# Performance work log

Measured on AMD Instinct MI355X. Metric: run time of the kernel, lower is better.

Reference implementation:

```python
import jax, jax.numpy as jnp
import numpy as np

B, CIN, H, W = 2, 3, 768, 768
CB = 32          # backbone out_channels (= channels_mid for heads)
ORDER = 5
MARGIN = 3.0     # ScaledTanh margin of refinement head


def _conv(x, w, b, pad):
    # x: [N,C,H,W], w: [O,I,kh,kw]
    y = jax.lax.conv_general_dilated(x, w, (1, 1), [(pad, pad), (pad, pad)],
                                     dimension_numbers=('NCHW', 'OIHW', 'NCHW'))
    return y + b[None, :, None, None]


def _readout(x, w1, b1, s, t, w2, b2, pad):
    # conv(k) -> batchnorm(eval, folded to scale/shift) -> relu -> dropout(eval=id) -> conv1x1
    h = _conv(x, w1, b1, pad)
    h = jax.nn.relu(h * s[None, :, None, None] + t[None, :, None, None])
    return _conv(h, w2, b2, 0)


def setup_inputs() -> dict:
    key = jax.random.key(0)
    ks = iter(jax.random.split(key, 16))
    def rn(shape, scale=0.05):
        return jax.random.normal(next(ks), shape, jnp.float32) * scale
    d = {'inputs': jax.random.normal(next(ks), (B, CIN, H, W), jnp.float32)}
    d['bb_w'] = rn((CB, CIN, 3, 3)); d['bb_b'] = jnp.zeros((CB,), jnp.float32)
    def head(name, k, cout):
        d[name + '_w1'] = rn((CB, CB, k, k)); d[name + '_b1'] = jnp.zeros((CB,), jnp.float32)
        d[name + '_s'] = jnp.ones((CB,), jnp.float32); d[name + '_t'] = jnp.zeros((CB,), jnp.float32)
        d[name + '_w2'] = rn((cout, CB, 1, 1)); d[name + '_b2'] = jnp.zeros((cout,), jnp.float32)
    head('score', 3, 2)
    head('loc', 7, 2)
    head('four', 7, ORDER * 4)
    head('ref', 7, 2)
    return d


def reference(inputs, bb_w, bb_b,
              score_w1, score_b1, score_s, score_t, score_w2, score_b2,
              loc_w1, loc_b1, loc_s, loc_t, loc_w2, loc_b2,
              four_w1, four_b1, four_s, four_t, four_w2, four_b2,
              ref_w1, ref_b1, ref_s, ref_t, ref_w2, ref_b2):
    # backbone (simple conv + relu; out_channels is an int so contour == refinement features)
    feats = jax.nn.relu(_conv(inputs, bb_w, bb_b, 1))
    scores = _readout(feats, score_w1, score_b1, score_s, score_t, score_w2, score_b2, 1)
    locations = _readout(feats, loc_w1, loc_b1, loc_s, loc_t, loc_w2, loc_b2, 3)
    fourier = _readout(feats, four_w1, four_b1, four_s, four_t, four_w2, four_b2, 3)
    # ReadOut final activation ScaledTanh(3.0), then CPNCore multiplies by internal margin 1.0;
    # feature HW == input HW (stride 1), so F.interpolate is a no-op.
    refinement = jnp.tanh(_readout(feats, ref_w1, ref_b1, ref_s, ref_t, ref_w2, ref_b2, 3)) * MARGIN
    return (scores, locations, refinement, fourier)
```

## Files before the change

### kernel.cpp

```cpp
#include <hip/hip_runtime.h>
#include <hip/hip_bf16.h>
#include <cmath>

#define HH 768
#define WW 768
#define HWSZ (768*768)

typedef __attribute__((ext_vector_type(8))) short bhalf8;
typedef __attribute__((ext_vector_type(4))) float f32x4;
typedef __attribute__((ext_vector_type(16))) float f32x16;

__device__ inline ushort f2bf(float f) {
  __hip_bfloat16 h = __float2bfloat16(f);
  return *reinterpret_cast<ushort*>(&h);
}

__global__ __launch_bounds__(256) void wxform_all_kernel(
    const float* __restrict__ w1S, const float* __restrict__ b1S,
    const float* __restrict__ sS,  const float* __restrict__ tS,
    const float* __restrict__ w1L, const float* __restrict__ b1L,
    const float* __restrict__ sL,  const float* __restrict__ tL,
    const float* __restrict__ w1F, const float* __restrict__ b1F,
    const float* __restrict__ sF,  const float* __restrict__ tF,
    const float* __restrict__ w1R, const float* __restrict__ b1R,
    const float* __restrict__ sR,  const float* __restrict__ tR,
    ushort* __restrict__ wT0, float* __restrict__ bb0, size_t wt_stride_elems)
{
  int h = blockIdx.y;
  const float *w1, *b1, *s, *t;
  int npos;
  if (h == 0)      { w1 = w1S; b1 = b1S; s = sS; t = tS; npos = 9;  }
  else if (h == 1) { w1 = w1L; b1 = b1L; s = sL; t = tL; npos = 49; }
  else if (h == 2) { w1 = w1F; b1 = b1F; s = sF; t = tF; npos = 49; }
  else             { w1 = w1R; b1 = b1R; s = sR; t = tR; npos = 49; }

  ushort* wT = wT0 + (size_t)h * wt_stride_elems;
  float*  bb = bb0 + h * 32;

  int i = blockIdx.x * 256 + threadIdx.x;
  if (i < npos * 1024) {
    int pos = i >> 10, mc = i & 1023, m = mc >> 5, c = mc & 31;
    wT[i] = f2bf(w1[(m * 32 + c) * npos + pos] * s[m]);
  }
  if (blockIdx.x == 0 && i < 32) bb[i] = b1[i] * s[i] + t[i];
}

__global__ __launch_bounds__(256) void backbone_kernel(
    const float* __restrict__ x, const float* __restrict__ w,
    const float* __restrict__ bias, ushort* __restrict__ feats)
{
  int p = blockIdx.x * 256 + threadIdx.x;
  int bb  = p / HWSZ;
  int rem = p - bb * HWSZ;
  int y   = rem / WW;
  int xx  = rem - y * WW;
  const float* xb = x + (size_t)bb * 3 * HWSZ;

  float v[3][3][3];
  #pragma unroll
  for (int c = 0; c < 3; c++)
    #pragma unroll
    for (int dy = 0; dy < 3; dy++)
      #pragma unroll
      for (int dx = 0; dx < 3; dx++) {
        int yy = y + dy - 1, xq = xx + dx - 1;
        v[c][dy][dx] = (yy >= 0 && yy < HH && xq >= 0 && xq < WW)
                         ? xb[(size_t)c * HWSZ + yy * WW + xq] : 0.f;
      }

  union { ushort u[32]; uint4 q[4]; } pk;
  #pragma unroll
  for (int o = 0; o < 32; o++) {
    float acc = bias[o];
    #pragma unroll
    for (int c = 0; c < 3; c++)
      #pragma unroll
      for (int dy = 0; dy < 3; dy++)
        #pragma unroll
        for (int dx = 0; dx < 3; dx++)
          acc = fmaf(w[((o * 3 + c) * 3 + dy) * 3 + dx], v[c][dy][dx], acc);
    pk.u[o] = f2bf(fmaxf(acc, 0.f));
  }
  uint4* dst = (uint4*)(feats + ((size_t)bb * HWSZ + rem) * 32);
  #pragma unroll
  for (int i = 0; i < 4; i++) dst[i] = pk.q[i];
}

template <int COUT, bool DO_TANH>
__device__ inline void head_epilogue(
    const f32x16 acc[2], const float* __restrict__ bbh,
    const float* __restrict__ w2, const float* __restrict__ b2,
    float* __restrict__ out_base, float* mid,
    int wv, int qr, int qc, int kg, int by, int bx, int bb)
{
  #pragma unroll
  for (int n = 0; n < 2; n++) {
    int pix = (wv * 4 + 2 * n + qr) * 16 + qc;
    #pragma unroll
    for (int rg = 0; rg < 4; rg++) {
      int m0 = 8 * rg + 4 * kg;
      f32x4 v;
      #pragma unroll
      for (int j = 0; j < 4; j++)
        v[j] = fmaxf(acc[n][rg * 4 + j] + bbh[m0 + j], 0.f);
      *(f32x4*)(mid + pix * 36 + m0) = v;
    }
  }
  __syncthreads();

  int t = threadIdx.x;
  float mv[32];
  #pragma unroll
  for (int j2 = 0; j2 < 8; j2++)
    *(f32x4*)(mv + 4 * j2) = *(const f32x4*)(mid + t * 36 + 4 * j2);

  int oy = by * 16 + (t >> 4), ox = bx * 16 + (t & 15);
  size_t opix = (size_t)oy * WW + ox;
  float* ob = out_base + (size_t)bb * COUT * HWSZ;
  #pragma unroll
  for (int oc = 0; oc < COUT; oc++) {
    float a2 = b2[oc];
    #pragma unroll
    for (int m = 0; m < 32; m++) a2 = fmaf(w2[oc * 32 + m], mv[m], a2);
    if (DO_TANH) a2 = tanhf(a2) * 3.0f;
    ob[(size_t)oc * HWSZ + opix] = a2;
  }
  __syncthreads();
}

__global__ __launch_bounds__(256, 2) void heads3_kernel(
    const ushort* __restrict__ feats,
    const ushort* __restrict__ wtL, const ushort* __restrict__ wtF,
    const ushort* __restrict__ wtR,
    const float* __restrict__ bbL, const float* __restrict__ bbF,
    const float* __restrict__ bbR,
    const float* __restrict__ w2L, const float* __restrict__ b2L,
    const float* __restrict__ w2F, const float* __restrict__ b2F,
    const float* __restrict__ w2R, const float* __restrict__ b2R,
    float* __restrict__ outL, float* __restrict__ outF, float* __restrict__ outR)
{
  __shared__ __align__(16) char smem[30976 + 28672];
  ushort* tile = (ushort*)smem;
  ushort* wrow = (ushort*)(smem + 30976);

  int bx = blockIdx.x % 48;
  int by = (blockIdx.x / 48) % 48;
  int bb = blockIdx.x / 2304;
  int x0 = bx * 16 - 3, y0 = by * 16 - 3;
  const ushort* fB = feats + (size_t)bb * HWSZ * 32;

  for (int p = threadIdx.x; p < 22 * 22; p += 256) {
    int r = p / 22, cl = p - r * 22;
    int yy = y0 + r, xx = x0 + cl;
    uint4 q0 = {0,0,0,0}, q1 = {0,0,0,0}, q2 = {0,0,0,0}, q3 = {0,0,0,0};
    if (yy >= 0 && yy < HH && xx >= 0 && xx < WW) {
      const uint4* src = (const uint4*)(fB + ((size_t)yy * WW + xx) * 32);
      q0 = src[0]; q1 = src[1]; q2 = src[2]; q3 = src[3];
    }
    ushort* dst = tile + r * 704 + cl * 8;
    *(uint4*)(dst +   0) = q0;
    *(uint4*)(dst + 176) = q1;
    *(uint4*)(dst + 352) = q2;
    *(uint4*)(dst + 528) = q3;
  }

  int l  = threadIdx.x & 63;
  int wv = threadIdx.x >> 6;
  int q  = l & 31;
  int kg = l >> 5;
  int qr = q >> 4, qc = q & 15;

  const ushort* pbB = tile + (wv * 4 + qr) * 704 + kg * 176 + qc * 8;
  const ushort* aB  = wrow + kg * 256 + q * 8;
  const ushort* aRb = wtR + q * 32 + kg * 8;

  f32x16 accL[2] = {};
  f32x16 accF[2] = {};
  f32x16 accR[2] = {};

  #pragma unroll 1
  for (int ky = 0; ky < 7; ky++) {
    {
      const ushort* rowL = wtL + ky * 7168;
      const ushort* rowF = wtF + ky * 7168;
      #pragma unroll
      for (int j = 0; j < 7; j++) {
        int c = j * 256 + (int)threadIdx.x;
        int h = (c >= 896) ? 1 : 0;
        int o = (c - h * 896) * 8;
        bhalf8 v = *(const bhalf8*)((h ? rowF : rowL) + o);
        int tap = o >> 10, rem = o & 1023;
        *(bhalf8*)(wrow + tap * 2048 + h * 1024 + ((rem >> 3) & 3) * 256 + (rem >> 5) * 8) = v;
      }
    }
    __syncthreads();

    const ushort* pbrow = pbB + ky * 704;
    const ushort* aR = aRb + ky * 7168;

    #pragma unroll
    for (int kx = 0; kx < 7; kx++) {
      bhalf8 fL[2], fF[2], fR[2];
      #pragma unroll
      for (int kh = 0; kh < 2; kh++) {
        fL[kh] = *(const bhalf8*)(aB + kx * 2048 +        kh * 512);
        fF[kh] = *(const bhalf8*)(aB + kx * 2048 + 1024 + kh * 512);
        fR[kh] = *(const bhalf8*)(aR + kx * 1024 + kh * 16);
      }
      bhalf8 bfr[2][2];
      #pragma unroll
      for (int n = 0; n < 2; n++)
        #pragma unroll
        for (int kh = 0; kh < 2; kh++)
          bfr[n][kh] = *(const bhalf8*)(pbrow + n * 1408 + kh * 352 + kx * 8);

      #pragma unroll
      for (int n = 0; n < 2; n++)
        #pragma unroll
        for (int kh = 0; kh < 2; kh++) {
          accL[n] = __builtin_amdgcn_mfma_f32_32x32x16_bf16(fL[kh], bfr[n][kh], accL[n], 0, 0, 0);
          accF[n] = __builtin_amdgcn_mfma_f32_32x32x16_bf16(fF[kh], bfr[n][kh], accF[n], 0, 0, 0);
          accR[n] = __builtin_amdgcn_mfma_f32_32x32x16_bf16(fR[kh], bfr[n][kh], accR[n], 0, 0, 0);
        }
    }
    __syncthreads();
  }

  float* mid = (float*)smem;

  head_epilogue<2,  false>(accL, bbL, w2L, b2L, outL, mid, wv, qr, qc, kg, by, bx, bb);
  head_epilogue<20, false>(accF, bbF, w2F, b2F, outF, mid, wv, qr, qc, kg, by, bx, bb);
  head_epilogue<2,  true >(accR, bbR, w2R, b2R, outR, mid, wv, qr, qc, kg, by, bx, bb);
}

__global__ __launch_bounds__(256, 4) void score_kernel(
    const ushort* __restrict__ feats,
    const ushort* __restrict__ wtS, const float* __restrict__ bbS,
    const float* __restrict__ w2S, const float* __restrict__ b2S,
    float* __restrict__ outS)
{
  constexpr int TW = 18, CPAD = 40;
  constexpr int SMEM_BYTES = 256 * 36 * 4;
  __shared__ __align__(16) char smem[SMEM_BYTES];
  ushort* tile = (ushort*)smem;

  int bx = blockIdx.x % 48;
  int by = (blockIdx.x / 48) % 48;
  int bb = blockIdx.x / 2304;
  int x0 = bx * 16 - 1, y0 = by * 16 - 1;
  const ushort* fB = feats + (size_t)bb * HWSZ * 32;

  for (int p = threadIdx.x; p < TW * TW; p += 256) {
    int py = p / TW, pxx = p % TW;
    int yy = y0 + py, xx = x0 + pxx;
    uint4 q0 = {0,0,0,0}, q1 = {0,0,0,0}, q2 = {0,0,0,0}, q3 = {0,0,0,0};
    if (yy >= 0 && yy < HH && xx >= 0 && xx < WW) {
      const uint4* src = (const uint4*)(fB + ((size_t)yy * WW + xx) * 32);
      q0 = src[0]; q1 = src[1]; q2 = src[2]; q3 = src[3];
    }
    uint4* dst = (uint4*)(tile + (size_t)p * CPAD);
    dst[0] = q0; dst[1] = q1; dst[2] = q2; dst[3] = q3;
  }
  __syncthreads();

  int l  = threadIdx.x & 63;
  int wv = threadIdx.x >> 6;
  int q  = l & 31;
  int kg = l >> 5;
  int qr = q >> 4, qc = q & 15;

  const ushort* pb = tile + ((wv * 4 + qr) * TW + qc) * CPAD + kg * 8;
  const int aoff = q * 32 + kg * 8;

  f32x16 acc[2] = {};

  #pragma unroll
  for (int ky = 0; ky < 3; ky++) {
    #pragma unroll
    for (int kx = 0; kx < 3; kx++) {
      const int tap = ky * 3 + kx;
      bhalf8 a0[2];
      #pragma unroll
      for (int kh = 0; kh < 2; kh++)
        a0[kh] = *(const bhalf8*)(wtS + tap * 1024 + aoff + kh * 16);
      #pragma unroll
      for (int n = 0; n < 2; n++) {
        #pragma unroll
        for (int kh = 0; kh < 2; kh++) {
          bhalf8 bf = *(const bhalf8*)(pb + (ky * TW + kx) * CPAD
                                          + n * 2 * TW * CPAD + kh * 16);
          acc[n] = __builtin_amdgcn_mfma_f32_32x32x16_bf16(a0[kh], bf, acc[n], 0, 0, 0);
        }
      }
    }
  }

  __syncthreads();
  float* mid = (float*)smem;
  head_epilogue<2, false>(acc, bbS, w2S, b2S, outS, mid, wv, qr, qc, kg, by, bx, bb);
}

extern "C" void kernel_launch(void* const* d_in, const int* in_sizes, int n_in,
                              void* d_out, int out_size, void* d_ws, size_t ws_size,
                              hipStream_t stream) {
  const float* input = (const float*)d_in[0];
  const float* bb_w  = (const float*)d_in[1];
  const float* bb_b  = (const float*)d_in[2];

  ushort* feats = (ushort*)d_ws;
  char* base = (char*)d_ws;
  const size_t FEATS_BYTES = (size_t)2 * HWSZ * 32 * 2;
  const size_t WT_STRIDE_E = 49 * 1024;
  ushort* wT0 = (ushort*)(base + FEATS_BYTES);
  float*  bb0 = (float*)(base + FEATS_BYTES + 4 * WT_STRIDE_E * 2);
  (void)out_size; (void)ws_size; (void)n_in; (void)in_sizes;

  float* out = (float*)d_out;
  float* outS = out;
  float* outL = out + (size_t)4  * HWSZ;
  float* outR = out + (size_t)8  * HWSZ;
  float* outF = out + (size_t)12 * HWSZ;

  dim3 wxgrid(196, 4);
  wxform_all_kernel<<<wxgrid, 256, 0, stream>>>(
      (const float*)d_in[3],  (const float*)d_in[4],  (const float*)d_in[5],  (const float*)d_in[6],
      (const float*)d_in[9],  (const float*)d_in[10], (const float*)d_in[11], (const float*)d_in[12],
      (const float*)d_in[15], (const float*)d_in[16], (const float*)d_in[17], (const float*)d_in[18],
      (const float*)d_in[21], (const float*)d_in[22], (const float*)d_in[23], (const float*)d_in[24],
      wT0, bb0, WT_STRIDE_E);

  backbone_kernel<<<4608, 256, 0, stream>>>(input, bb_w, bb_b, feats);

  const ushort* wtS = wT0 + 0 * WT_STRIDE_E;
  const ushort* wtL = wT0 + 1 * WT_STRIDE_E;
  const ushort* wtF = wT0 + 2 * WT_STRIDE_E;
  const ushort* wtR = wT0 + 3 * WT_STRIDE_E;

  const int GRID = 2 * 48 * 48;

  heads3_kernel<<<GRID, 256, 0, stream>>>(
      feats, wtL, wtF, wtR,
      bb0 + 32, bb0 + 64, bb0 + 96,
      (const float*)d_in[13], (const float*)d_in[14],
      (const float*)d_in[19], (const float*)d_in[20],
      (const float*)d_in[25], (const float*)d_in[26],
      outL, outF, outR);

  score_kernel<<<GRID, 256, 0, stream>>>(
      feats, wtS, bb0 + 0,
      (const float*)d_in[7], (const float*)d_in[8], outS);
}
```

Baseline: 414.9 us.

## Widen heads3 tile to 16x32 with 512 threads and bf16 epilogue staging

The fused 7x7 heads kernel now processes a 16x32 output tile per block with 512 threads, so each halo load and each weight-row staging serves twice as many pixels. Only six of the seven taps per weight row are staged in LDS, with precomputed copy addresses; the seventh tap is read directly from global memory so the staging buffer fits beside the larger input tile. The intermediate buffer before the 1x1 conv is stored as bf16 to save LDS, which adds rounding error. The launch bound changes to (512,4), which may cap registers tightly enough to spill the 96 accumulator floats per lane.

```diff
diff --git a/kernel.cpp b/kernel.cpp
--- a/kernel.cpp
+++ b/kernel.cpp
@@ -13,6 +13,9 @@
 __device__ inline ushort f2bf(float f) {
   __hip_bfloat16 h = __float2bfloat16(f);
   return *reinterpret_cast<ushort*>(&h);
+}
+__device__ inline float bf2f(ushort u) {
+  union { unsigned int i; float f; } v; v.i = ((unsigned int)u) << 16; return v.f;
 }
 
 __global__ __launch_bounds__(256) void wxform_all_kernel(
@@ -87,23 +90,26 @@
 }
 
 template <int COUT, bool DO_TANH>
-__device__ inline void head_epilogue(
+__device__ inline void head_epilogue3(
     const f32x16 acc[2], const float* __restrict__ bbh,
     const float* __restrict__ w2, const float* __restrict__ b2,
-    float* __restrict__ out_base, float* mid,
+    float* __restrict__ out_base, ushort* mid,
     int wv, int qr, int qc, int kg, int by, int bx, int bb)
 {
   #pragma unroll
   for (int n = 0; n < 2; n++) {
-    int pix = (wv * 4 + 2 * n + qr) * 16 + qc;
+    int px = (2 * wv + qr) * 32 + n * 16 + qc;
     #pragma unroll
     for (int rg = 0; rg < 4; rg++) {
       int m0 = 8 * rg + 4 * kg;
-      f32x4 v;
+      ushort u[4];
       #pragma unroll
       for (int j = 0; j < 4; j++)
-        v[j] = fmaxf(acc[n][rg * 4 + j] + bbh[m0 + j], 0.f);
-      *(f32x4*)(mid + pix * 36 + m0) = v;
+        u[j] = f2bf(fmaxf(acc[n][rg * 4 + j] + bbh[m0 + j], 0.f));
+      uint2 pkv;
+      pkv.x = (unsigned int)u[0] | ((unsigned int)u[1] << 16);
+      pkv.y = (unsigned int)u[2] | ((unsigned int)u[3] << 16);
+      *(uint2*)(mid + px * 36 + m0) = pkv;
     }
   }
   __syncthreads();
@@ -111,10 +117,14 @@
   int t = threadIdx.x;
   float mv[32];
   #pragma unroll
-  for (int j2 = 0; j2 < 8; j2++)
-    *(f32x4*)(mv + 4 * j2) = *(const f32x4*)(mid + t * 36 + 4 * j2);
-
-  int oy = by * 16 + (t >> 4), ox = bx * 16 + (t & 15);
+  for (int j = 0; j < 8; j++) {
+    uint2 r = *(const uint2*)(mid + t * 36 + j * 4);
+    mv[j * 4 + 0] = bf2f((ushort)(r.x & 0xffff));
+    mv[j * 4 + 1] = bf2f((ushort)(r.x >> 16));
+    mv[j * 4 + 2] = bf2f((ushort)(r.y & 0xffff));
+    mv[j * 4 + 3] = bf2f((ushort)(r.y >> 16));
+  }
+  int oy = by * 16 + (t >> 5), ox = bx * 32 + (t & 31);
   size_t opix = (size_t)oy * WW + ox;
   float* ob = out_base + (size_t)bb * COUT * HWSZ;
   #pragma unroll
@@ -128,7 +138,7 @@
   __syncthreads();
 }
 
-__global__ __launch_bounds__(256, 2) void heads3_kernel(
+__global__ __launch_bounds__(512, 4) void heads3_kernel(
     const ushort* __restrict__ feats,
     const ushort* __restrict__ wtL, const ushort* __restrict__ wtF,
     const ushort* __restrict__ wtR,
@@ -139,40 +149,55 @@
     const float* __restrict__ w2R, const float* __restrict__ b2R,
     float* __restrict__ outL, float* __restrict__ outF, float* __restrict__ outR)
 {
-  __shared__ __align__(16) char smem[30976 + 28672];
+  __shared__ __align__(16) char smem[53504 + 24576];
   ushort* tile = (ushort*)smem;
-  ushort* wrow = (ushort*)(smem + 30976);
-
-  int bx = blockIdx.x % 48;
-  int by = (blockIdx.x / 48) % 48;
-  int bb = blockIdx.x / 2304;
-  int x0 = bx * 16 - 3, y0 = by * 16 - 3;
+  ushort* wrow = (ushort*)(smem + 53504);
+
+  int bx = blockIdx.x % 24;
+  int by = (blockIdx.x / 24) % 48;
+  int bb = blockIdx.x / 1152;
+  int x0 = bx * 32 - 3, y0 = by * 16 - 3;
   const ushort* fB = feats + (size_t)bb * HWSZ * 32;
 
-  for (int p = threadIdx.x; p < 22 * 22; p += 256) {
-    int r = p / 22, cl = p - r * 22;
+  for (int p = threadIdx.x; p < 22 * 38; p += 512) {
+    int r = p / 38, cl = p - r * 38;
     int yy = y0 + r, xx = x0 + cl;
     uint4 q0 = {0,0,0,0}, q1 = {0,0,0,0}, q2 = {0,0,0,0}, q3 = {0,0,0,0};
     if (yy >= 0 && yy < HH && xx >= 0 && xx < WW) {
       const uint4* src = (const uint4*)(fB + ((size_t)yy * WW + xx) * 32);
       q0 = src[0]; q1 = src[1]; q2 = src[2]; q3 = src[3];
     }
-    ushort* dst = tile + r * 704 + cl * 8;
+    ushort* dst = tile + r * 1216 + cl * 8;
     *(uint4*)(dst +   0) = q0;
-    *(uint4*)(dst + 176) = q1;
-    *(uint4*)(dst + 352) = q2;
-    *(uint4*)(dst + 528) = q3;
-  }
-
-  int l  = threadIdx.x & 63;
-  int wv = threadIdx.x >> 6;
+    *(uint4*)(dst + 304) = q1;
+    *(uint4*)(dst + 608) = q2;
+    *(uint4*)(dst + 912) = q3;
+  }
+
+  int tid = threadIdx.x;
+  int l  = tid & 63;
+  int wv = tid >> 6;
   int q  = l & 31;
   int kg = l >> 5;
   int qr = q >> 4, qc = q & 15;
 
-  const ushort* pbB = tile + (wv * 4 + qr) * 704 + kg * 176 + qc * 8;
+  const ushort* pb  = tile + (2 * wv + qr) * 1216 + kg * 304 + qc * 8;
   const ushort* aB  = wrow + kg * 256 + q * 8;
-  const ushort* aRb = wtR + q * 32 + kg * 8;
+  const ushort* aGL = wtL + q * 32 + kg * 8;
+  const ushort* aGF = wtF + q * 32 + kg * 8;
+  const ushort* aGR = wtR + q * 32 + kg * 8;
+
+  int st_kx[3], st_src_off[3];
+  const ushort* st_base[3];
+  #pragma unroll
+  for (int j = 0; j < 3; j++) {
+    int idx = j * 512 + tid;
+    int kx = idx >> 8, rem = idx & 255;
+    int h = rem >> 7, g = (rem >> 5) & 3, m = rem & 31;
+    st_kx[j] = idx;
+    st_base[j] = h ? wtF : wtL;
+    st_src_off[j] = kx * 1024 + m * 32 + g * 8;
+  }
 
   f32x16 accL[2] = {};
   f32x16 accF[2] = {};
@@ -180,31 +205,29 @@
 
   #pragma unroll 1
   for (int ky = 0; ky < 7; ky++) {
-    {
-      const ushort* rowL = wtL + ky * 7168;
-      const ushort* rowF = wtF + ky * 7168;
-      #pragma unroll
-      for (int j = 0; j < 7; j++) {
-        int c = j * 256 + (int)threadIdx.x;
-        int h = (c >= 896) ? 1 : 0;
-        int o = (c - h * 896) * 8;
-        bhalf8 v = *(const bhalf8*)((h ? rowF : rowL) + o);
-        int tap = o >> 10, rem = o & 1023;
-        *(bhalf8*)(wrow + tap * 2048 + h * 1024 + ((rem >> 3) & 3) * 256 + (rem >> 5) * 8) = v;
-      }
-    }
     __syncthreads();
-
-    const ushort* pbrow = pbB + ky * 704;
-    const ushort* aR = aRb + ky * 7168;
+    #pragma unroll
+    for (int j = 0; j < 3; j++) {
+      bhalf8 v = *(const bhalf8*)(st_base[j] + ky * 7168 + st_src_off[j]);
+      *(bhalf8*)(wrow + st_kx[j] * 8) = v;
+    }
+    __syncthreads();
+
+    const ushort* pbrow = pb + ky * 1216;
+    const ushort* aR = aGR + ky * 7168;
 
     #pragma unroll
     for (int kx = 0; kx < 7; kx++) {
       bhalf8 fL[2], fF[2], fR[2];
       #pragma unroll
       for (int kh = 0; kh < 2; kh++) {
-        fL[kh] = *(const bhalf8*)(aB + kx * 2048 +        kh * 512);
-        fF[kh] = *(const bhalf8*)(aB + kx * 2048 + 1024 + kh * 512);
+        if (kx < 6) {
+          fL[kh] = *(const bhalf8*)(aB + kx * 2048 +        kh * 512);
+          fF[kh] = *(const bhalf8*)(aB + kx * 2048 + 1024 + kh * 512);
+        } else {
+          fL[kh] = *(const bhalf8*)(aGL + ky * 7168 + 6144 + kh * 16);
+          fF[kh] = *(const bhalf8*)(aGF + ky * 7168 + 6144 + kh * 16);
+        }
         fR[kh] = *(const bhalf8*)(aR + kx * 1024 + kh * 16);
       }
       bhalf8 bfr[2][2];
@@ -212,7 +235,7 @@
       for (int n = 0; n < 2; n++)
         #pragma unroll
         for (int kh = 0; kh < 2; kh++)
-          bfr[n][kh] = *(const bhalf8*)(pbrow + n * 1408 + kh * 352 + kx * 8);
+          bfr[n][kh] = *(const bhalf8*)(pbrow + kh * 608 + n * 128 + kx * 8);
 
       #pragma unroll
       for (int n = 0; n < 2; n++)
@@ -223,14 +246,56 @@
           accR[n] = __builtin_amdgcn_mfma_f32_32x32x16_bf16(fR[kh], bfr[n][kh], accR[n], 0, 0, 0);
         }
     }
-    __syncthreads();
-  }
-
-  float* mid = (float*)smem;
-
-  head_epilogue<2,  false>(accL, bbL, w2L, b2L, outL, mid, wv, qr, qc, kg, by, bx, bb);
-  head_epilogue<20, false>(accF, bbF, w2F, b2F, outF, mid, wv, qr, qc, kg, by, bx, bb);
-  head_epilogue<2,  true >(accR, bbR, w2R, b2R, outR, mid, wv, qr, qc, kg, by, bx, bb);
+  }
+
+  __syncthreads();
+  ushort* mid = (ushort*)smem;
+
+  head_epilogue3<2,  false>(accL, bbL, w2L, b2L, outL, mid, wv, qr, qc, kg, by, bx, bb);
+  head_epilogue3<20, false>(accF, bbF, w2F, b2F, outF, mid, wv, qr, qc, kg, by, bx, bb);
+  head_epilogue3<2,  true >(accR, bbR, w2R, b2R, outR, mid, wv, qr, qc, kg, by, bx, bb);
+}
+
+typedef __attribute__((ext_vector_type(4))) float f32x4b;
+template <int COUT, bool DO_TANH>
+__device__ inline void head_epilogue_s(
+    const f32x16 acc[2], const float* __restrict__ bbh,
+    const float* __restrict__ w2, const float* __restrict__ b2,
+    float* __restrict__ out_base, float* mid,
+    int wv, int qr, int qc, int kg, int by, int bx, int bb)
+{
+  #pragma unroll
+  for (int n = 0; n < 2; n++) {
+    int pix = (wv * 4 + 2 * n + qr) * 16 + qc;
+    #pragma unroll
+    for (int rg = 0; rg < 4; rg++) {
+      int m0 = 8 * rg + 4 * kg;
+      f32x4 v;
+      #pragma unroll
+      for (int j = 0; j < 4; j++)
+        v[j] = fmaxf(acc[n][rg * 4 + j] + bbh[m0 + j], 0.f);
+      *(f32x4*)(mid + pix * 36 + m0) = v;
+    }
+  }
+  __syncthreads();
+
+  int t = threadIdx.x;
+  float mv[32];
+  #pragma unroll
+  for (int j2 = 0; j2 < 8; j2++)
+    *(f32x4*)(mv + 4 * j2) = *(const f32x4*)(mid + t * 36 + 4 * j2);
+
+  int oy = by * 16 + (t >> 4), ox = bx * 16 + (t & 15);
+  size_t opix = (size_t)oy * WW + ox;
+  float* ob = out_base + (size_t)bb * COUT * HWSZ;
+  #pragma unroll
+  for (int oc = 0; oc < COUT; oc++) {
+    float a2 = b2[oc];
+    #pragma unroll
+    for (int m = 0; m < 32; m++) a2 = fmaf(w2[oc * 32 + m], mv[m], a2);
+    if (DO_TANH) a2 = tanhf(a2) * 3.0f;
+    ob[(size_t)oc * HWSZ + opix] = a2;
+  }
 }
 
 __global__ __launch_bounds__(256, 4) void score_kernel(
@@ -297,7 +362,7 @@
 
   __syncthreads();
   float* mid = (float*)smem;
-  head_epilogue<2, false>(acc, bbS, w2S, b2S, outS, mid, wv, qr, qc, kg, by, bx, bb);
+  head_epilogue_s<2, false>(acc, bbS, w2S, b2S, outS, mid, wv, qr, qc, kg, by, bx, bb);
 }
 
 extern "C" void kernel_launch(void* const* d_in, const int* in_sizes, int n_in,
@@ -336,9 +401,7 @@
   const ushort* wtF = wT0 + 2 * WT_STRIDE_E;
   const ushort* wtR = wT0 + 3 * WT_STRIDE_E;
 
-  const int GRID = 2 * 48 * 48;
-
-  heads3_kernel<<<GRID, 256, 0, stream>>>(
+  heads3_kernel<<<2 * 48 * 24, 512, 0, stream>>>(
       feats, wtL, wtF, wtR,
       bb0 + 32, bb0 + 64, bb0 + 96,
       (const float*)d_in[13], (const float*)d_in[14],
@@ -346,7 +409,7 @@
       (const float*)d_in[25], (const float*)d_in[26],
       outL, outF, outR);
 
-  score_kernel<<<GRID, 256, 0, stream>>>(
+  score_kernel<<<2 * 48 * 48, 256, 0, stream>>>(
       feats, wtS, bb0 + 0,
       (const float*)d_in[7], (const float*)d_in[8], outS);
 }
```

Result: slower. 435.1 us (+4.9%).
